# Optimization experiments

Measured on AMD Instinct MI355X. Metric: run time of the kernel, lower is better.

The kernel has to match this reference:

```python
import jax, jax.numpy as jnp
import numpy as np

T, B, D = 512, 64, 1024


def setup_inputs() -> dict:
    key = jax.random.key(0)
    k1, k2, k3, k4 = jax.random.split(key, 4)
    scale = 1.0 / np.sqrt(D)
    x = jax.random.normal(k1, (T, B, D), dtype=jnp.float32)
    resets = jax.random.randint(k2, (T, B), 0, 2) > 0  # bool reset mask per step
    Wi = jax.random.normal(k3, (D, 3 * D), dtype=jnp.float32) * scale  # [ir|iz|in]
    bi = jnp.zeros((3 * D,), dtype=jnp.float32)
    Wh = jax.random.normal(k4, (D, 3 * D), dtype=jnp.float32) * scale  # [hr|hz|hn]
    bhn = jnp.zeros((D,), dtype=jnp.float32)  # bias only on hn gate (flax GRUCell)
    return {"x": x, "Wi": Wi, "bi": bi, "Wh": Wh, "bhn": bhn, "resets": resets}


def reference(x, Wi, bi, Wh, bhn, resets):
    """Scan of flax nn.GRUCell with reset-masked carry. x: [T,B,D], resets: [T,B] bool."""
    Bsz, Dh = x.shape[1], x.shape[2]

    def step(h, inp):
        xt, rt = inp  # xt: [B,D], rt: [B]
        h = jnp.where(rt[:, None], jnp.zeros_like(h), h)  # reset carry to zeros
        gi = xt @ Wi + bi          # [B,3D]
        gh = h @ Wh                # [B,3D] (no bias for r,z in flax GRUCell)
        ir_, iz_, in_ = jnp.split(gi, 3, axis=-1)
        hr_, hz_, hn_ = jnp.split(gh, 3, axis=-1)
        r = jax.nn.sigmoid(ir_ + hr_)
        z = jax.nn.sigmoid(iz_ + hz_)
        n = jnp.tanh(in_ + r * (hn_ + bhn))
        h_new = (1.0 - z) * n + z * h
        return h_new, h_new

    h0 = jnp.zeros((Bsz, Dh), dtype=x.dtype)  # flax initialize_carry default: zeros
    _, ys = jax.lax.scan(step, h0, (x, resets))
    return ys  # [T,B,D]
```

## Files before the change

kernel.cpp:

```cpp
#include <hip/hip_runtime.h>


typedef __attribute__((ext_vector_type(8))) short short8;
typedef __attribute__((ext_vector_type(4))) float f32x4;
typedef __attribute__((ext_vector_type(4))) unsigned int u32x4;

#define DEV static __device__ __forceinline__

constexpr int TT = 512, BB = 64, DD = 1024, TD = 3072;

constexpr size_t WS_BAR = 256;
constexpr size_t WS_H = 8192;
constexpr size_t HPLANE = (size_t)BB * DD * 2;
constexpr size_t WS_NEED = WS_H + 4 * HPLANE;

DEV unsigned short f2bf(float f) {
    unsigned u = __builtin_bit_cast(unsigned, f);
    u += 0x7FFFu + ((u >> 16) & 1u);
    return (unsigned short)(u >> 16);
}
DEV float bf2f(unsigned short s) { return __builtin_bit_cast(float, ((unsigned)s) << 16); }

DEV void ld16c(u32x4& r, const unsigned* p) {
    asm volatile("global_load_dwordx4 %0, %1, off sc0 sc1" : "=v"(r) : "v"(p));
}
DEV void ld16(u32x4& r, const unsigned* p) {
    asm volatile("global_load_dwordx4 %0, %1, off" : "=v"(r) : "v"(p));
}
DEV void ld8u(unsigned& r, const unsigned char* p) {
    asm volatile("global_load_ubyte %0, %1, off" : "=v"(r) : "v"(p));
}
DEV void vm0() {
    asm volatile("s_waitcnt vmcnt(0)" ::: "memory");
    __builtin_amdgcn_sched_barrier(0);
}
#define WAITN(n) do { asm volatile("s_waitcnt vmcnt(" #n ")" ::: "memory"); \
                      __builtin_amdgcn_sched_barrier(0); } while (0)

__global__ void pack_x_kernel(const float* __restrict__ x, unsigned* __restrict__ outw) {
    const size_t gid = (size_t)blockIdx.x * 256 + threadIdx.x;
    const size_t e0 = gid * 8;
    const unsigned t = (unsigned)(e0 >> 16);
    const unsigned p = (unsigned)(e0 & 65535u);
    const unsigned r = p >> 10, d = p & 1023u;
    const unsigned m = r >> 4, lr = r & 15u;
    f32x4 a = *(const f32x4*)(x + e0);
    f32x4 b = *(const f32x4*)(x + e0 + 4);
    u32x4 wh, wl;
#pragma unroll
    for (int j = 0; j < 2; ++j) {
        unsigned short h0 = f2bf(a[2 * j]), h1 = f2bf(a[2 * j + 1]);
        wh[j] = (unsigned)h0 | ((unsigned)h1 << 16);
        wl[j] = (unsigned)f2bf(a[2 * j] - bf2f(h0)) | ((unsigned)f2bf(a[2 * j + 1] - bf2f(h1)) << 16);
        unsigned short g0 = f2bf(b[2 * j]), g1 = f2bf(b[2 * j + 1]);
        wh[2 + j] = (unsigned)g0 | ((unsigned)g1 << 16);
        wl[2 + j] = (unsigned)f2bf(b[2 * j] - bf2f(g0)) | ((unsigned)f2bf(b[2 * j + 1] - bf2f(g1)) << 16);
    }
    unsigned* base = outw + (size_t)t * 65536u + m * 16384u + ((lr * 1024u + d) >> 1);
    *(u32x4*)base = wh;
    *(u32x4*)(base + 8192u) = wl;
}

__global__ void prep_kernel(const unsigned char* __restrict__ resets, unsigned char* __restrict__ ws) {
    const int bid = blockIdx.x, tid = threadIdx.x;
    if (bid < 256) {
        ((unsigned*)(ws + WS_H))[bid * 256 + tid] = 0u;
    } else {
        unsigned* w32 = (unsigned*)ws;
        for (int i = tid; i < 2048; i += 256) w32[i] = 0u;
        __shared__ int ca, cb, cc;
        if (tid == 0) { ca = 0; cb = 0; cc = 0; }
        __syncthreads();
        int la = 0, lb = 0, lc = 0;
        for (int o = tid * 16; o < tid * 16 + 16; ++o) {
            unsigned char v = resets[o];
            if (v) {
                if ((o & 3) == 0) la = 1; else lb = 1;
                if ((o & 7) == 4) lc = 1;
            }
        }
        if (la) atomicOr(&ca, 1);
        if (lb) atomicOr(&cb, 1);
        if (lc) atomicOr(&cc, 1);
        __syncthreads();
        if (tid == 0) {
            unsigned stride, boff = 0;
            if (ca && cb)       { stride = 1; }
            else if (!ca && cb) { stride = 4; boff = 3; }
            else if (ca && cc)  { stride = 4; }
            else if (ca)        { stride = 8; }
            else                { stride = 4; }
            w32[0] = stride; w32[1] = boff;
        }
    }
}

__launch_bounds__(512, 1)
__global__ void gru_kernel(const float* __restrict__ Wi, const float* __restrict__ bi,
                           const float* __restrict__ Wh, const float* __restrict__ bhn,
                           const unsigned char* __restrict__ resets,
                           float* __restrict__ out, unsigned char* __restrict__ ws) {
    const int tid = threadIdx.x;
    const int wg = blockIdx.x;
    const int lane = tid & 63;
    const int kw = tid >> 6;
    const int mgrp = wg >> 6;
    const int cg = wg & 63;
    const int c0 = cg * 16;

    unsigned* bar = (unsigned*)(ws + WS_BAR) + mgrp * 256;
    unsigned* rep = &bar[((cg * 4 + kw) & 7) * 32];
    const unsigned rstride = ((const unsigned*)ws)[0];
    const unsigned rboff   = ((const unsigned*)ws)[1];

    unsigned short* h_hi[2] = {(unsigned short*)(ws + WS_H),
                               (unsigned short*)(ws + WS_H + 2 * HPLANE)};
    unsigned short* h_lo[2] = {(unsigned short*)(ws + WS_H + HPLANE),
                               (unsigned short*)(ws + WS_H + 3 * HPLANE)};
    unsigned* outw = (unsigned*)out;

    const int lrow = lane & 15;
    const int lk = (lane >> 4) * 8;

    short8 bih[3][4], bhh[3][4], bhl[3][4];
#pragma unroll
    for (int nt = 0; nt < 3; ++nt) {
        const int col = nt * DD + c0 + lrow;
#pragma unroll
        for (int kt = 0; kt < 4; ++kt) {
            const int kb = kw * 128 + kt * 32 + lk;
            short8 a, c, d;
#pragma unroll
            for (int j = 0; j < 8; ++j) {
                float wi = Wi[(size_t)(kb + j) * TD + col];
                a[j] = (short)f2bf(wi);
                float wh = Wh[(size_t)(kb + j) * TD + col];
                unsigned short h2 = f2bf(wh);
                c[j] = (short)h2;
                d[j] = (short)f2bf(wh - bf2f(h2));
            }
            bih[nt][kt] = a; bhh[nt][kt] = c; bhl[nt][kt] = d;
        }
    }

    const int eb = (tid & 255) >> 4, ej = tid & 15;
    const int brow = mgrp * 16 + eb;
    const int ce = c0 + ej;
    const float bi_r = bi[ce], bi_z = bi[DD + ce], bi_n = bi[2 * DD + ce];
    const float bh_n = bhn[ce];
    float h_local = 0.f;
    float ys_prev = 0.f;

    const unsigned xlidx = (unsigned)(lrow * 1024 + kw * 128 + lk);
    const unsigned xwbase = (unsigned)mgrp * 16384u + (xlidx >> 1);
    const unsigned hidx = (unsigned)((mgrp * 16 + lrow) * 1024 + kw * 128 + lk);
    const size_t r64 = (size_t)64 * rstride;
    const size_t roffb = (size_t)brow * rstride + rboff;

    __shared__ float pgi[8][3][16][18];
    __shared__ float pgh[8][3][16][18];
    const int prow = (lane >> 4) * 4;

    {
        const unsigned* xpl = outw;
        u32x4 xf[8];
#pragma unroll
        for (int kt = 0; kt < 4; ++kt) {
            ld16(xf[2 * kt],     xpl + xwbase + kt * 16);
            ld16(xf[2 * kt + 1], xpl + xwbase + 8192u + kt * 16);
        }
        vm0();
        f32x4 ai[3] = {f32x4{0}, f32x4{0}, f32x4{0}};
#pragma unroll
        for (int kt = 0; kt < 4; ++kt) {
            short8 xh = __builtin_bit_cast(short8, xf[2 * kt]);
            short8 xl = __builtin_bit_cast(short8, xf[2 * kt + 1]);
#pragma unroll
            for (int nt = 0; nt < 3; ++nt)
                ai[nt] = __builtin_amdgcn_mfma_f32_16x16x32_bf16(xh, bih[nt][kt], ai[nt], 0, 0, 0);
#pragma unroll
            for (int nt = 0; nt < 3; ++nt)
                ai[nt] = __builtin_amdgcn_mfma_f32_16x16x32_bf16(xl, bih[nt][kt], ai[nt], 0, 0, 0);
        }
#pragma unroll
        for (int s = 0; s < 3; ++s)
#pragma unroll
            for (int i = 0; i < 4; ++i)
                pgi[kw][s][prow + i][lrow] = ai[s][i];
        __syncthreads();
    }

    for (int t = 0; t < TT; ++t) {
        if (t) {
            const unsigned target = 256u * (unsigned)t;
            int guard = 1 << 20;
            unsigned s;
            do {
                s = 0;
#pragma unroll
                for (int r2 = 0; r2 < 8; ++r2)
                    s += __hip_atomic_load(&bar[r2 * 32], __ATOMIC_RELAXED, __HIP_MEMORY_SCOPE_AGENT);
            } while (s < target && --guard);
        }
        __builtin_amdgcn_sched_barrier(0);

        unsigned rsv;
        ld8u(rsv, resets + roffb + (size_t)((t + 1 < TT) ? (t + 1) : (TT - 1)) * r64);

        const int cur = t & 1;
        const unsigned* hhp = (const unsigned*)h_hi[cur];
        const unsigned* hlp = (const unsigned*)h_lo[cur];
        u32x4 hf[8];
#pragma unroll
        for (int kt = 0; kt < 4; ++kt) {
            ld16c(hf[2 * kt],     hhp + ((hidx + kt * 32) >> 1));
            ld16c(hf[2 * kt + 1], hlp + ((hidx + kt * 32) >> 1));
        }

        const unsigned* xpl = outw + (size_t)((t + 1 < TT) ? (t + 1) : (TT - 1)) * 65536u;
        u32x4 xf[8];
#pragma unroll
        for (int kt = 0; kt < 4; ++kt) {
            ld16(xf[2 * kt],     xpl + xwbase + kt * 16);
            ld16(xf[2 * kt + 1], xpl + xwbase + 8192u + kt * 16);
        }

        float g0 = 0.f, g1 = 0.f, g2 = 0.f;
        if (tid < 256) {
#pragma unroll
            for (int k = 0; k < 8; ++k) {
                g0 += pgi[k][0][eb][ej];
                g1 += pgi[k][1][eb][ej];
                g2 += pgi[k][2][eb][ej];
            }
        }

        f32x4 ag[3] = {f32x4{0}, f32x4{0}, f32x4{0}};
        __builtin_amdgcn_s_setprio(1);
        {
            WAITN(14);
            short8 hh = __builtin_bit_cast(short8, hf[0]);
            short8 hl = __builtin_bit_cast(short8, hf[1]);
#pragma unroll
            for (int nt = 0; nt < 3; ++nt) {
                ag[nt] = __builtin_amdgcn_mfma_f32_16x16x32_bf16(hh, bhh[nt][0], ag[nt], 0, 0, 0);
                ag[nt] = __builtin_amdgcn_mfma_f32_16x16x32_bf16(hl, bhh[nt][0], ag[nt], 0, 0, 0);
                ag[nt] = __builtin_amdgcn_mfma_f32_16x16x32_bf16(hh, bhl[nt][0], ag[nt], 0, 0, 0);
            }
        }
        {
            WAITN(12);
            short8 hh = __builtin_bit_cast(short8, hf[2]);
            short8 hl = __builtin_bit_cast(short8, hf[3]);
#pragma unroll
            for (int nt = 0; nt < 3; ++nt) {
                ag[nt] = __builtin_amdgcn_mfma_f32_16x16x32_bf16(hh, bhh[nt][1], ag[nt], 0, 0, 0);
                ag[nt] = __builtin_amdgcn_mfma_f32_16x16x32_bf16(hl, bhh[nt][1], ag[nt], 0, 0, 0);
                ag[nt] = __builtin_amdgcn_mfma_f32_16x16x32_bf16(hh, bhl[nt][1], ag[nt], 0, 0, 0);
            }
        }
        {
            WAITN(10);
            short8 hh = __builtin_bit_cast(short8, hf[4]);
            short8 hl = __builtin_bit_cast(short8, hf[5]);
#pragma unroll
            for (int nt = 0; nt < 3; ++nt) {
                ag[nt] = __builtin_amdgcn_mfma_f32_16x16x32_bf16(hh, bhh[nt][2], ag[nt], 0, 0, 0);
                ag[nt] = __builtin_amdgcn_mfma_f32_16x16x32_bf16(hl, bhh[nt][2], ag[nt], 0, 0, 0);
                ag[nt] = __builtin_amdgcn_mfma_f32_16x16x32_bf16(hh, bhl[nt][2], ag[nt], 0, 0, 0);
            }
        }
        {
            WAITN(8);
            short8 hh = __builtin_bit_cast(short8, hf[6]);
            short8 hl = __builtin_bit_cast(short8, hf[7]);
#pragma unroll
            for (int nt = 0; nt < 3; ++nt) {
                ag[nt] = __builtin_amdgcn_mfma_f32_16x16x32_bf16(hh, bhh[nt][3], ag[nt], 0, 0, 0);
                ag[nt] = __builtin_amdgcn_mfma_f32_16x16x32_bf16(hl, bhh[nt][3], ag[nt], 0, 0, 0);
                ag[nt] = __builtin_amdgcn_mfma_f32_16x16x32_bf16(hh, bhl[nt][3], ag[nt], 0, 0, 0);
            }
        }
        __builtin_amdgcn_s_setprio(0);

#pragma unroll
        for (int s = 0; s < 3; ++s)
#pragma unroll
            for (int i = 0; i < 4; ++i)
                pgh[kw][s][prow + i][lrow] = ag[s][i];
        __syncthreads();

        if (tid < 256) {
            float h0 = 0.f, h1 = 0.f, h2 = 0.f;
#pragma unroll
            for (int k = 0; k < 8; ++k) {
                h0 += pgh[k][0][eb][ej];
                h1 += pgh[k][1][eb][ej];
                h2 += pgh[k][2][eb][ej];
            }
            float r = 1.f / (1.f + __expf(-(g0 + bi_r + h0)));
            float z = 1.f / (1.f + __expf(-(g1 + bi_z + h1)));
            float pre = g2 + bi_n + r * (h2 + bh_n);
            float e2 = __expf(2.f * pre);
            float n = 1.f - 2.f / (e2 + 1.f);
            float hnew = (1.f - z) * n + z * h_local;

            if (t) out[(size_t)(t - 1) * 65536u + brow * DD + ce] = ys_prev;
            ys_prev = hnew;

            if (t < TT - 1) {
                float heff = (rsv != 0u) ? 0.f : hnew;
                h_local = heff;
                unsigned short ph = f2bf(heff);
                unsigned short pl = f2bf(heff - bf2f(ph));
                __hip_atomic_store(h_hi[cur ^ 1] + brow * DD + ce, ph,
                                   __ATOMIC_RELAXED, __HIP_MEMORY_SCOPE_AGENT);
                __hip_atomic_store(h_lo[cur ^ 1] + brow * DD + ce, pl,
                                   __ATOMIC_RELAXED, __HIP_MEMORY_SCOPE_AGENT);
            }
        }

        if (kw < 4) {
            vm0();
            if (lane == 0 && t < TT - 1)
                __hip_atomic_fetch_add(rep, 1u, __ATOMIC_RELAXED, __HIP_MEMORY_SCOPE_AGENT);
        }

        if (t < TT - 1) {
            WAITN(0);
            f32x4 ai[3] = {f32x4{0}, f32x4{0}, f32x4{0}};
#pragma unroll
            for (int kt = 0; kt < 4; ++kt) {
                short8 xh = __builtin_bit_cast(short8, xf[2 * kt]);
                short8 xl = __builtin_bit_cast(short8, xf[2 * kt + 1]);
#pragma unroll
                for (int nt = 0; nt < 3; ++nt)
                    ai[nt] = __builtin_amdgcn_mfma_f32_16x16x32_bf16(xh, bih[nt][kt], ai[nt], 0, 0, 0);
#pragma unroll
                for (int nt = 0; nt < 3; ++nt)
                    ai[nt] = __builtin_amdgcn_mfma_f32_16x16x32_bf16(xl, bih[nt][kt], ai[nt], 0, 0, 0);
            }
#pragma unroll
            for (int s = 0; s < 3; ++s)
#pragma unroll
                for (int i = 0; i < 4; ++i)
                    pgi[kw][s][prow + i][lrow] = ai[s][i];
            __syncthreads();
        }
    }

    if (tid < 256)
        out[(size_t)(TT - 1) * 65536u + brow * DD + ce] = ys_prev;
}

extern "C" void kernel_launch(void* const* d_in, const int* in_sizes, int n_in,
                              void* d_out, int out_size, void* d_ws, size_t ws_size,
                              hipStream_t stream) {
    const float* x = (const float*)d_in[0];
    const float* Wi = (const float*)d_in[1];
    const float* bi = (const float*)d_in[2];
    const float* Wh = (const float*)d_in[3];
    const float* bhn = (const float*)d_in[4];
    const unsigned char* resets = (const unsigned char*)d_in[5];
    float* out = (float*)d_out;
    unsigned char* ws = (unsigned char*)d_ws;

    if (ws_size < WS_NEED) return;

    hipLaunchKernelGGL(pack_x_kernel, dim3(16384), dim3(256), 0, stream, x, (unsigned*)out);
    hipLaunchKernelGGL(prep_kernel, dim3(257), dim3(256), 0, stream, resets, ws);

    void* args[] = {(void*)&Wi, (void*)&bi, (void*)&Wh, (void*)&bhn,
                    (void*)&resets, (void*)&out, (void*)&ws};
    hipError_t err = hipLaunchCooperativeKernel((const void*)gru_kernel, dim3(256), dim3(512),
                                                args, 0, stream);
    if (err != hipSuccess) {
        hipLaunchKernelGGL(gru_kernel, dim3(256), dim3(512), 0, stream,
                           Wi, bi, Wh, bhn, resets, out, ws);
    }
}
```

Before: 2.724 ms.

## Replace counter-sum grid barrier with per-wave epoch flags and transpose LDS partials

The inter-workgroup barrier changes from atomic fetch-add counters summed over eight replicas to per-wave monotonic epoch flags. Each wave stores its step number, and consumers poll all 256 flags in parallel across lanes, using a wave vote to check completion. This removes atomic RMW contention and serialized summation from the per-step critical path. Separately, the LDS partial-sum arrays are transposed and padded to 17 to change bank mapping on writes and reads. It risks more polling traffic, since each lane loads four flags per spin.

Measured after the change: 3.048 ms. +11.9%, slower.

```diff
diff --git a/kernel.cpp b/kernel.cpp
--- a/kernel.cpp
+++ b/kernel.cpp
@@ -9,7 +9,7 @@
 
 constexpr int TT = 512, BB = 64, DD = 1024, TD = 3072;
 
-constexpr size_t WS_BAR = 256;
+constexpr size_t WS_FLAGS = 256;
 constexpr size_t WS_H = 8192;
 constexpr size_t HPLANE = (size_t)BB * DD * 2;
 constexpr size_t WS_NEED = WS_H + 4 * HPLANE;
@@ -108,8 +108,7 @@
     const int cg = wg & 63;
     const int c0 = cg * 16;
 
-    unsigned* bar = (unsigned*)(ws + WS_BAR) + mgrp * 256;
-    unsigned* rep = &bar[((cg * 4 + kw) & 7) * 32];
+    unsigned* fl = (unsigned*)(ws + WS_FLAGS) + mgrp * 256;
     const unsigned rstride = ((const unsigned*)ws)[0];
     const unsigned rboff   = ((const unsigned*)ws)[1];
 
@@ -157,8 +156,8 @@
     const size_t r64 = (size_t)64 * rstride;
     const size_t roffb = (size_t)brow * rstride + rboff;
 
-    __shared__ float pgi[8][3][16][18];
-    __shared__ float pgh[8][3][16][18];
+    __shared__ float pgi[8][3][16][17];
+    __shared__ float pgh[8][3][16][17];
     const int prow = (lane >> 4) * 4;
 
     {
@@ -186,26 +185,31 @@
         for (int s = 0; s < 3; ++s)
 #pragma unroll
             for (int i = 0; i < 4; ++i)
-                pgi[kw][s][prow + i][lrow] = ai[s][i];
+                pgi[kw][s][lrow][prow + i] = ai[s][i];
         __syncthreads();
+        if (kw < 4 && lane == 0)
+            __hip_atomic_store(&fl[cg * 4 + kw], 1u, __ATOMIC_RELAXED, __HIP_MEMORY_SCOPE_AGENT);
     }
 
     for (int t = 0; t < TT; ++t) {
-        if (t) {
-            const unsigned target = 256u * (unsigned)t;
+        {
+            const unsigned tgt = (unsigned)(t + 1);
             int guard = 1 << 20;
-            unsigned s;
-            do {
-                s = 0;
-#pragma unroll
-                for (int r2 = 0; r2 < 8; ++r2)
-                    s += __hip_atomic_load(&bar[r2 * 32], __ATOMIC_RELAXED, __HIP_MEMORY_SCOPE_AGENT);
-            } while (s < target && --guard);
+            while (true) {
+                unsigned f0 = __hip_atomic_load(&fl[lane * 4 + 0], __ATOMIC_RELAXED, __HIP_MEMORY_SCOPE_AGENT);
+                unsigned f1 = __hip_atomic_load(&fl[lane * 4 + 1], __ATOMIC_RELAXED, __HIP_MEMORY_SCOPE_AGENT);
+                unsigned f2 = __hip_atomic_load(&fl[lane * 4 + 2], __ATOMIC_RELAXED, __HIP_MEMORY_SCOPE_AGENT);
+                unsigned f3 = __hip_atomic_load(&fl[lane * 4 + 3], __ATOMIC_RELAXED, __HIP_MEMORY_SCOPE_AGENT);
+                int ok = (f0 >= tgt) & (f1 >= tgt) & (f2 >= tgt) & (f3 >= tgt);
+                if (__all(ok) || --guard == 0) break;
+            }
         }
         __builtin_amdgcn_sched_barrier(0);
 
+        const int tn = (t + 1 < TT) ? (t + 1) : (TT - 1);
+
         unsigned rsv;
-        ld8u(rsv, resets + roffb + (size_t)((t + 1 < TT) ? (t + 1) : (TT - 1)) * r64);
+        ld8u(rsv, resets + roffb + (size_t)tn * r64);
 
         const int cur = t & 1;
         const unsigned* hhp = (const unsigned*)h_hi[cur];
@@ -216,8 +220,7 @@
             ld16c(hf[2 * kt],     hhp + ((hidx + kt * 32) >> 1));
             ld16c(hf[2 * kt + 1], hlp + ((hidx + kt * 32) >> 1));
         }
-
-        const unsigned* xpl = outw + (size_t)((t + 1 < TT) ? (t + 1) : (TT - 1)) * 65536u;
+        const unsigned* xpl = outw + (size_t)tn * 65536u;
         u32x4 xf[8];
 #pragma unroll
         for (int kt = 0; kt < 4; ++kt) {
@@ -229,9 +232,9 @@
         if (tid < 256) {
 #pragma unroll
             for (int k = 0; k < 8; ++k) {
-                g0 += pgi[k][0][eb][ej];
-                g1 += pgi[k][1][eb][ej];
-                g2 += pgi[k][2][eb][ej];
+                g0 += pgi[k][0][ej][eb];
+                g1 += pgi[k][1][ej][eb];
+                g2 += pgi[k][2][ej][eb];
             }
         }
 
@@ -287,16 +290,16 @@
         for (int s = 0; s < 3; ++s)
 #pragma unroll
             for (int i = 0; i < 4; ++i)
-                pgh[kw][s][prow + i][lrow] = ag[s][i];
+                pgh[kw][s][lrow][prow + i] = ag[s][i];
         __syncthreads();
 
         if (tid < 256) {
             float h0 = 0.f, h1 = 0.f, h2 = 0.f;
 #pragma unroll
             for (int k = 0; k < 8; ++k) {
-                h0 += pgh[k][0][eb][ej];
-                h1 += pgh[k][1][eb][ej];
-                h2 += pgh[k][2][eb][ej];
+                h0 += pgh[k][0][ej][eb];
+                h1 += pgh[k][1][ej][eb];
+                h2 += pgh[k][2][ej][eb];
             }
             float r = 1.f / (1.f + __expf(-(g0 + bi_r + h0)));
             float z = 1.f / (1.f + __expf(-(g1 + bi_z + h1)));
@@ -323,7 +326,8 @@
         if (kw < 4) {
             vm0();
             if (lane == 0 && t < TT - 1)
-                __hip_atomic_fetch_add(rep, 1u, __ATOMIC_RELAXED, __HIP_MEMORY_SCOPE_AGENT);
+                __hip_atomic_store(&fl[cg * 4 + kw], (unsigned)(t + 2),
+                                   __ATOMIC_RELAXED, __HIP_MEMORY_SCOPE_AGENT);
         }
 
         if (t < TT - 1) {
@@ -344,7 +348,7 @@
             for (int s = 0; s < 3; ++s)
 #pragma unroll
                 for (int i = 0; i < 4; ++i)
-                    pgi[kw][s][prow + i][lrow] = ai[s][i];
+                    pgi[kw][s][lrow][prow + i] = ai[s][i];
             __syncthreads();
         }
     }
```
